# Kernel optimization log

Hardware: AMD Instinct MI355X
Metric: run time of the kernel (lower is better)

The kernel has to match this reference:

```python
import math
import jax, jax.numpy as jnp
import numpy as np

NUM_LAYERS = 2  # init arg num_layers
MASK_FILL = 1e-10  # non-standard fill used by the original (not -inf)


def _pos_encoding(L, D):
    # Matches torch PositionalEncoding buffer (dropout is identity in eval).
    pos = np.arange(L, dtype=np.float32)[:, None]
    div = np.exp(np.arange(0, D, 2, dtype=np.float32) * (-math.log(10000.0) / D))
    pe = np.zeros((L, D), dtype=np.float32)
    pe[:, 0::2] = np.sin(pos * div)
    pe[:, 1::2] = np.cos(pos * div)
    return jnp.asarray(pe)


def setup_inputs() -> dict:
    B, L, D = 1024, 100, 512
    key = jax.random.key(0)
    ks = jax.random.split(key, 6)
    x = jax.random.normal(ks[0], (B, L, D), dtype=jnp.float32)
    text_len = jax.random.randint(ks[1], (B,), 1, L + 1)  # in [1, L]
    scale = 1.0 / np.sqrt(2 * D)  # stand-in for orthogonal init
    W_r = jax.random.normal(ks[2], (2 * D, D), dtype=jnp.float32) * scale
    W_u = jax.random.normal(ks[3], (2 * D, D), dtype=jnp.float32) * scale
    W_o = jax.random.normal(ks[4], (2 * D, D), dtype=jnp.float32) * scale
    b = jnp.zeros((D,), dtype=jnp.float32)
    return {"x": x, "text_len": text_len, "W_r": W_r, "b_r": b,
            "W_u": W_u, "b_u": b, "W_o": W_o, "b_o": b}


def reference(x, text_len, W_r, b_r, W_u, b_u, W_o, b_o):
    B, L, D = x.shape
    pe = _pos_encoding(L, D)  # [L, D]
    valid = jnp.arange(L)[None, :] < text_len[:, None]          # [B, L]
    mask = valid[:, :, None] & valid[:, None, :]                 # [B, L, L]
    for _ in range(NUM_LAYERS):
        xp = x + pe  # PE (dropout identity in eval), applied to both sides
        score = jnp.einsum('bld,bmd->blm', xp, xp)               # [B, L, L]
        score = jnp.where(mask, score, MASK_FILL)
        attn = jax.nn.softmax(score, axis=2)
        message = jnp.einsum('blm,bmd->bld', attn, x)            # [B, L, D]
        # ConvGRU cell (prev_state = x): gates are Linear on last dim
        si = jnp.concatenate([message, x], axis=-1)              # [B, L, 2D]
        update = jax.nn.sigmoid(si @ W_u + b_u)
        reset = jax.nn.sigmoid(si @ W_r + b_r)
        so = jnp.concatenate([message, x * reset], axis=-1)
        cand = jnp.tanh(so @ W_o + b_o)
        x = x * (1.0 - update) + cand * update
    # mean_with_lens pooling
    lenf = text_len.astype(x.dtype)
    seq_emb = jnp.sum(x * valid[:, :, None].astype(x.dtype), axis=1) / lenf[:, None]
    return x, seq_emb
```

## Files before the change

kernel.cpp:

```cpp
#include <hip/hip_runtime.h>
#include <hip/hip_bf16.h>

#define B_ 1024
#define L_ 100
#define D_ 512
#define LP 128
#define ROWS (B_*L_)
#define XELEMS ((size_t)ROWS*D_)
#define HB 512
#define HR (HB*L_)
#define CATW 1536

typedef __attribute__((ext_vector_type(8))) short short8;
typedef __attribute__((ext_vector_type(4))) float f32x4;
typedef unsigned long long ull_t;

__device__ __forceinline__ short f2bf(float f) {
    __hip_bfloat16 h = __float2bfloat16(f);
    return *reinterpret_cast<short*>(&h);
}
__device__ __forceinline__ float bf2f(short s) {
    __hip_bfloat16 h = *reinterpret_cast<__hip_bfloat16*>(&s);
    return __bfloat162float(h);
}

__device__ __forceinline__ void cp16(void* lds, const void* g) {
    __builtin_amdgcn_global_load_lds(
        (const __attribute__((address_space(1))) unsigned int*)g,
        (__attribute__((address_space(3))) unsigned int*)lds, 16, 0, 0);
}

__device__ __forceinline__ f32x4 mfma16(short8 a, short8 b, f32x4 c) {
    return __builtin_amdgcn_mfma_f32_16x16x32_bf16(a, b, c, 0, 0, 0);
}

__global__ __launch_bounds__(256) void pe_kernel(float* __restrict__ pe) {
    int idx = blockIdx.x * 256 + threadIdx.x;
    if (idx >= L_ * D_) return;
    int l = idx >> 9;
    int d = idx & 511;
    int i = d >> 1;
    float div = __expf((float)(2 * i) * (-9.210340371976184f / 512.0f));
    float angle = (float)l * div;
    pe[idx] = (d & 1) ? __cosf(angle) : __sinf(angle);
}

__global__ __launch_bounds__(256) void cvtw_kernel(const float* __restrict__ W,
                                                   __hip_bfloat16* __restrict__ Wt) {
    int idx = blockIdx.x * 256 + threadIdx.x;
    int n = idx >> 10, k = idx & 1023;
    Wt[idx] = __float2bfloat16(W[(size_t)k * D_ + n]);
}

template<int BF16IN>
__global__ __launch_bounds__(256) void attn_kernel(
    const float* __restrict__ x, const float* __restrict__ pe,
    const int* __restrict__ text_len, __hip_bfloat16* __restrict__ xTb,
    __hip_bfloat16* __restrict__ cat, int bh)
{
    __shared__ __align__(16) char sm[16384 + 32768];
    char* XP = sm;
    char* P  = sm + 16384;
    const int bl = blockIdx.x;
    const int b = bh * HB + bl;
    const int len = text_len[b];
    const int tid = threadIdx.x;
    const int w = tid >> 6, g = (tid >> 4) & 3, cl = tid & 15;
    const int lane = tid & 63;
    const float* xb = x + (size_t)b * L_ * D_;
    __hip_bfloat16* xTg = xTb + (size_t)bl * D_ * LP;

    {
        __hip_bfloat16 (*t)[66] = (__hip_bfloat16 (*)[66])XP;
        for (int d0 = 0; d0 < D_; d0 += 64) {
            for (int l0 = 0; l0 < LP; l0 += 64) {
                int l_loc = tid >> 2;
                int dq = tid & 3;
                int l = l0 + l_loc;
                #pragma unroll
                for (int i = 0; i < 4; ++i) {
                    int d_loc = (dq * 4 + i) * 4;
                    if constexpr (BF16IN) {
                        ull_t u = 0ull;
                        if (l < L_)
                            u = *(const ull_t*)(cat + ((size_t)bl * L_ + l) * CATW + 512 + d0 + d_loc);
                        union { ull_t u; short s[4]; } pk;
                        pk.u = u;
                        t[l_loc][d_loc + 0] = *reinterpret_cast<__hip_bfloat16*>(&pk.s[0]);
                        t[l_loc][d_loc + 1] = *reinterpret_cast<__hip_bfloat16*>(&pk.s[1]);
                        t[l_loc][d_loc + 2] = *reinterpret_cast<__hip_bfloat16*>(&pk.s[2]);
                        t[l_loc][d_loc + 3] = *reinterpret_cast<__hip_bfloat16*>(&pk.s[3]);
                    } else {
                        float4 v = (l < L_) ? *(const float4*)(xb + (size_t)l * D_ + d0 + d_loc)
                                            : make_float4(0.f, 0.f, 0.f, 0.f);
                        short s0 = f2bf(v.x), s1 = f2bf(v.y), s2 = f2bf(v.z), s3 = f2bf(v.w);
                        t[l_loc][d_loc + 0] = *reinterpret_cast<__hip_bfloat16*>(&s0);
                        t[l_loc][d_loc + 1] = *reinterpret_cast<__hip_bfloat16*>(&s1);
                        t[l_loc][d_loc + 2] = *reinterpret_cast<__hip_bfloat16*>(&s2);
                        t[l_loc][d_loc + 3] = *reinterpret_cast<__hip_bfloat16*>(&s3);
                        if (l < L_) {
                            union { short s[4]; ull_t u; } pk;
                            pk.s[0] = s0; pk.s[1] = s1; pk.s[2] = s2; pk.s[3] = s3;
                            *(ull_t*)(cat + ((size_t)bl * L_ + l) * CATW + 512 + d0 + d_loc) = pk.u;
                        }
                    }
                }
                __syncthreads();
                int dl = tid >> 2, seg = tid & 3;
                short8 lo, hi;
                #pragma unroll
                for (int j = 0; j < 8; ++j) {
                    __hip_bfloat16 a = t[seg * 16 + j][dl];
                    __hip_bfloat16 bswap = t[seg * 16 + 8 + j][dl];
                    lo[j] = *reinterpret_cast<short*>(&a);
                    hi[j] = *reinterpret_cast<short*>(&bswap);
                }
                __hip_bfloat16* dst = xTg + (size_t)(d0 + dl) * LP + l0 + seg * 16;
                *(short8*)dst = lo;
                *(short8*)(dst + 8) = hi;
                __syncthreads();
            }
        }
    }

    f32x4 accS[2][8];
    const f32x4 fz = {0.f, 0.f, 0.f, 0.f};
    #pragma unroll
    for (int i = 0; i < 2; ++i)
        #pragma unroll
        for (int j = 0; j < 8; ++j) accS[i][j] = fz;

    for (int kc = 0; kc < D_; kc += 64) {
        #pragma unroll
        for (int i = 0; i < 4; ++i) {
            int c = tid + 256 * i;
            int row = c >> 3, k8d = c & 7;
            int k = kc + 8 * (k8d ^ (row & 7));
            if (row < L_) {
                const float* pp = pe + row * D_ + k;
                float4 b0 = *(const float4*)pp, b1 = *(const float4*)(pp + 4);
                short8 xv = *(const short8*)(cat + ((size_t)bl * L_ + row) * CATW + 512 + k);
                short8 h;
                h[0] = f2bf(bf2f(xv[0]) + b0.x); h[1] = f2bf(bf2f(xv[1]) + b0.y);
                h[2] = f2bf(bf2f(xv[2]) + b0.z); h[3] = f2bf(bf2f(xv[3]) + b0.w);
                h[4] = f2bf(bf2f(xv[4]) + b1.x); h[5] = f2bf(bf2f(xv[5]) + b1.y);
                h[6] = f2bf(bf2f(xv[6]) + b1.z); h[7] = f2bf(bf2f(xv[7]) + b1.w);
                *(short8*)(XP + row * 128 + 16 * k8d) = h;
            } else if (kc == 0) {
                short8 h;
                #pragma unroll
                for (int q = 0; q < 8; ++q) h[q] = 0;
                *(short8*)(XP + row * 128 + 16 * k8d) = h;
            }
        }
        __syncthreads();
        #pragma unroll
        for (int kt = 0; kt < 2; ++kt) {
            short8 a[2];
            #pragma unroll
            for (int rt = 0; rt < 2; ++rt) {
                int r = 32 * w + 16 * rt + cl;
                a[rt] = *(const short8*)(XP + r * 128 + ((16 * g + 64 * kt) ^ ((r & 7) << 4)));
            }
            #pragma unroll
            for (int ct = 0; ct < 8; ++ct) {
                int m = 16 * ct + cl;
                short8 bb = *(const short8*)(XP + m * 128 + ((16 * g + 64 * kt) ^ ((m & 7) << 4)));
                accS[0][ct] = mfma16(a[0], bb, accS[0][ct]);
                accS[1][ct] = mfma16(a[1], bb, accS[1][ct]);
            }
        }
        __syncthreads();
    }

    #pragma unroll
    for (int rt = 0; rt < 2; ++rt) {
        #pragma unroll
        for (int reg = 0; reg < 4; ++reg) {
            int rl = 32 * w + 16 * rt + 4 * g + reg;
            float s[8];
            #pragma unroll
            for (int ct = 0; ct < 8; ++ct) {
                int col = 16 * ct + cl;
                float v = accS[rt][ct][reg];
                if (col >= L_) v = -INFINITY;
                else if (rl >= len || col >= len) v = 1e-10f;
                s[ct] = v;
            }
            float mx = s[0];
            #pragma unroll
            for (int ct = 1; ct < 8; ++ct) mx = fmaxf(mx, s[ct]);
            mx = fmaxf(mx, __shfl_xor(mx, 1));
            mx = fmaxf(mx, __shfl_xor(mx, 2));
            mx = fmaxf(mx, __shfl_xor(mx, 4));
            mx = fmaxf(mx, __shfl_xor(mx, 8));
            float e[8], sum = 0.f;
            #pragma unroll
            for (int ct = 0; ct < 8; ++ct) { e[ct] = __expf(s[ct] - mx); sum += e[ct]; }
            sum += __shfl_xor(sum, 1);
            sum += __shfl_xor(sum, 2);
            sum += __shfl_xor(sum, 4);
            sum += __shfl_xor(sum, 8);
            float inv = 1.f / sum;
            #pragma unroll
            for (int ct = 0; ct < 8; ++ct) {
                int col = 16 * ct + cl;
                *(short*)(P + rl * 256 + ((col * 2) ^ ((rl & 7) << 4))) = f2bf(e[ct] * inv);
            }
        }
    }

    const __hip_bfloat16* xT = xTg;
    char* TW = XP + w * 4096;
    for (int nc = 0; nc < 4; ++nc) {
        f32x4 accM[2][8];
        #pragma unroll
        for (int i = 0; i < 2; ++i)
            #pragma unroll
            for (int j = 0; j < 8; ++j) accM[i][j] = fz;
        #pragma unroll
        for (int kt = 0; kt < 4; ++kt) {
            short8 a[2];
            #pragma unroll
            for (int rt = 0; rt < 2; ++rt) {
                int r = 32 * w + 16 * rt + cl;
                a[rt] = *(const short8*)(P + r * 256 + ((16 * g + 64 * kt) ^ ((r & 7) << 4)));
            }
            #pragma unroll
            for (int nt = 0; nt < 8; ++nt) {
                int d = nc * 128 + nt * 16 + cl;
                short8 bb = *(const short8*)(xT + (size_t)d * LP + 8 * g + 32 * kt);
                accM[0][nt] = mfma16(a[0], bb, accM[0][nt]);
                accM[1][nt] = mfma16(a[1], bb, accM[1][nt]);
            }
        }
        #pragma unroll
        for (int rt = 0; rt < 2; ++rt) {
            #pragma unroll
            for (int nt = 0; nt < 8; ++nt) {
                #pragma unroll
                for (int reg = 0; reg < 4; ++reg) {
                    int rloc = 4 * g + reg;
                    int cc = nt * 16 + cl;
                    *(short*)(TW + rloc * 256 + ((2 * cc) ^ ((rloc & 15) << 4))) =
                        f2bf(accM[rt][nt][reg]);
                }
            }
            asm volatile("s_waitcnt lgkmcnt(0)" ::: "memory");
            __builtin_amdgcn_sched_barrier(0);
            {
                int r4 = lane >> 4;
                int c16 = lane & 15;
                #pragma unroll
                for (int it = 0; it < 4; ++it) {
                    int rloc = it * 4 + r4;
                    int rl = 32 * w + 16 * rt + rloc;
                    if (rl < L_) {
                        int byte = (c16 * 16) ^ ((rloc & 15) << 4);
                        short8 v = *(const short8*)(TW + rloc * 256 + byte);
                        int d = nc * 128 + c16 * 8;
                        *(short8*)(cat + ((size_t)bl * L_ + rl) * CATW + d) = v;
                    }
                }
            }
            asm volatile("s_waitcnt lgkmcnt(0)" ::: "memory");
            __builtin_amdgcn_sched_barrier(0);
        }
    }
}

template<int MODE, int LAST>
__global__ __launch_bounds__(256) void gemm_gates(
    const __hip_bfloat16* __restrict__ cat,
    const __hip_bfloat16* __restrict__ Wt,
    const float* __restrict__ bias0, const float* __restrict__ bias1,
    __hip_bfloat16* __restrict__ upd,
    __hip_bfloat16* __restrict__ catw,
    float* __restrict__ xdst)
{
    __shared__ __align__(16) char sm[49152];
    const int tid = threadIdx.x;
    const int w = tid >> 6, g = (tid >> 4) & 3, cl = tid & 15;
    const int wr = w >> 1, wc = w & 1;
    constexpr int NY = (MODE == 0) ? 8 : 4;
    const int cpx = gridDim.x >> 3;
    const int bid = blockIdx.x;
    const int swz = (bid & 7) * cpx + (bid >> 3);
    const int bx = swz / NY, by = swz % NY;
    const size_t R0 = (size_t)bx * 128;
    const int col0 = by * 128;

    int srow[2], skoff[2];
    #pragma unroll
    for (int i = 0; i < 2; ++i) {
        int p = tid + 256 * i;
        int R = p >> 3, s = p & 7;
        int u = s ^ (R & 7);
        srow[i] = 2 * R + (u >> 2);
        skoff[i] = (u & 3) * 16;
    }

    auto stage = [&](int t, char* buf) {
        const int kc = t * 32;
        const int ka = (MODE == 0) ? kc : (t < 16 ? kc : kc + 512);
        #pragma unroll
        for (int i = 0; i < 2; ++i) {
            int p = tid + 256 * i;
            const char* gA = (const char*)(cat + (R0 + srow[i]) * CATW + ka) + skoff[i];
            cp16(buf + p * 16, gA);
        }
        #pragma unroll
        for (int i = 0; i < 2; ++i) {
            int p = tid + 256 * i;
            const char* gB = (const char*)(Wt + (size_t)(col0 + srow[i]) * 1024 + kc) + skoff[i];
            cp16(buf + 8192 + p * 16, gB);
        }
    };

    f32x4 acc[4][4];
    const f32x4 fz = {0.f, 0.f, 0.f, 0.f};
    #pragma unroll
    for (int i = 0; i < 4; ++i)
        #pragma unroll
        for (int j = 0; j < 4; ++j) acc[i][j] = fz;

    stage(0, sm);
    stage(1, sm + 16384);
    #pragma unroll 1
    for (int t = 0; t < 32; ++t) {
        char* buf = sm + 16384 * (t % 3);
        if (t < 31) asm volatile("s_waitcnt vmcnt(4)" ::: "memory");
        else        asm volatile("s_waitcnt vmcnt(0)" ::: "memory");
        __builtin_amdgcn_sched_barrier(0);
        __builtin_amdgcn_s_barrier();
        if (t + 2 < 32)
            stage(t + 2, sm + 16384 * ((t + 2) % 3));

        short8 aA[4], bb[4];
        #pragma unroll
        for (int rt = 0; rt < 4; ++rt) {
            int r = wr * 64 + rt * 16 + cl;
            int Rr = r >> 1;
            int sA = (((r & 1) << 2) + g) ^ (Rr & 7);
            aA[rt] = *(const short8*)(buf + Rr * 128 + 16 * sA);
        }
        #pragma unroll
        for (int ct = 0; ct < 4; ++ct) {
            int n = wc * 64 + ct * 16 + cl;
            int Rn = n >> 1;
            int sB = (((n & 1) << 2) + g) ^ (Rn & 7);
            bb[ct] = *(const short8*)(buf + 8192 + Rn * 128 + 16 * sB);
        }
        __builtin_amdgcn_s_setprio(1);
        #pragma unroll
        for (int rt = 0; rt < 4; ++rt)
            #pragma unroll
            for (int ct = 0; ct < 4; ++ct)
                acc[rt][ct] = mfma16(aA[rt], bb[ct], acc[rt][ct]);
        __builtin_amdgcn_s_setprio(0);
    }

    char* T = sm;
    #pragma unroll
    for (int ct = 0; ct < 4; ++ct) {
        int c = wc * 64 + ct * 16 + cl;
        int colg = col0 + c;
        float bb = (MODE == 0) ? ((col0 < 512) ? bias0[colg] : bias1[colg - 512])
                               : bias0[colg];
        #pragma unroll
        for (int rt = 0; rt < 4; ++rt) {
            #pragma unroll
            for (int reg = 0; reg < 4; ++reg) {
                int r = wr * 64 + rt * 16 + g * 4 + reg;
                float z = acc[rt][ct][reg] + bb;
                float v;
                if (MODE == 0) v = 1.f / (1.f + __expf(-z));
                else           v = 1.f - 2.f * __fdividef(1.f, 1.f + __expf(2.f * z));
                *(short*)(T + r * 256 + ((2 * c) ^ ((r & 15) << 4))) = f2bf(v);
            }
        }
    }
    __syncthreads();
    {
        const int rr = tid >> 4;
        const int c16 = tid & 15;
        #pragma unroll
        for (int it = 0; it < 8; ++it) {
            int r = it * 16 + rr;
            const size_t grow = R0 + r;
            int byte = (c16 * 16) ^ ((r & 15) << 4);
            short8 v = *(const short8*)(T + r * 256 + byte);
            int colg = col0 + c16 * 8;
            if (MODE == 0) {
                if (col0 < 512) {
                    *(short8*)(upd + grow * D_ + colg) = v;
                } else {
                    int c2 = colg - 512;
                    short8 xv = *(const short8*)(cat + grow * CATW + 512 + c2);
                    short8 o;
                    #pragma unroll
                    for (int q = 0; q < 8; ++q)
                        o[q] = f2bf(bf2f(xv[q]) * bf2f(v[q]));
                    *(short8*)(catw + grow * CATW + 1024 + c2) = o;
                }
            } else {
                short8 uv = *(const short8*)(upd + grow * D_ + colg);
                short8 xv = *(const short8*)(cat + grow * CATW + 512 + colg);
                if (LAST) {
                    float o[8];
                    #pragma unroll
                    for (int q = 0; q < 8; ++q) {
                        float u = bf2f(uv[q]), x_ = bf2f(xv[q]), cd = bf2f(v[q]);
                        o[q] = x_ + u * (cd - x_);
                    }
                    *(float4*)(xdst + grow * D_ + colg)     = make_float4(o[0], o[1], o[2], o[3]);
                    *(float4*)(xdst + grow * D_ + colg + 4) = make_float4(o[4], o[5], o[6], o[7]);
                } else {
                    short8 o;
                    #pragma unroll
                    for (int q = 0; q < 8; ++q) {
                        float u = bf2f(uv[q]), x_ = bf2f(xv[q]), cd = bf2f(v[q]);
                        o[q] = f2bf(x_ + u * (cd - x_));
                    }
                    *(short8*)(catw + grow * CATW + 512 + colg) = o;
                }
            }
        }
    }
}

__global__ __launch_bounds__(256) void pool_kernel(
    const float* __restrict__ x, const int* __restrict__ text_len,
    float* __restrict__ seq)
{
    int b = blockIdx.x;
    int len = text_len[b];
    float invlen = 1.f / (float)len;
    const float* xb = x + (size_t)b * L_ * D_;
    for (int d = threadIdx.x; d < D_; d += 256) {
        float acc = 0.f;
        for (int l = 0; l < len; ++l)
            acc += xb[(size_t)l * D_ + d];
        seq[(size_t)b * D_ + d] = acc * invlen;
    }
}

extern "C" void kernel_launch(void* const* d_in, const int* in_sizes, int n_in,
                              void* d_out, int out_size, void* d_ws, size_t ws_size,
                              hipStream_t stream) {
    const float* x_in = (const float*)d_in[0];
    const int* text_len = (const int*)d_in[1];
    const float* W_r = (const float*)d_in[2];
    const float* b_r = (const float*)d_in[3];
    const float* W_u = (const float*)d_in[4];
    const float* b_u = (const float*)d_in[5];
    const float* W_o = (const float*)d_in[6];
    const float* b_o = (const float*)d_in[7];

    float* xwork = (float*)d_out;
    float* seq_out = (float*)d_out + XELEMS;

    char* ws = (char*)d_ws;
    float* pe            = (float*)ws;
    __hip_bfloat16* WurT = (__hip_bfloat16*)(ws + 204800);
    __hip_bfloat16* WoT  = (__hip_bfloat16*)(ws + 2301952);
    __hip_bfloat16* cat  = (__hip_bfloat16*)(ws + 3350528);
    char* unionR         = ws + 160636928ull;
    __hip_bfloat16* xTb  = (__hip_bfloat16*)unionR;
    __hip_bfloat16* upd  = (__hip_bfloat16*)unionR;

    pe_kernel<<<(L_ * D_ + 255) / 256, 256, 0, stream>>>(pe);
    cvtw_kernel<<<2048, 256, 0, stream>>>(W_u, WurT);
    cvtw_kernel<<<2048, 256, 0, stream>>>(W_r, WurT + 512 * 1024);
    cvtw_kernel<<<2048, 256, 0, stream>>>(W_o, WoT);

    for (int h = 0; h < 2; ++h) {
        float* xdh = xwork + (size_t)h * HR * D_;
        attn_kernel<0><<<HB, 256, 0, stream>>>(x_in, pe, text_len, xTb, cat, h);
        gemm_gates<0, 0><<<3200, 256, 0, stream>>>(cat, WurT, b_u, b_r, upd, cat, nullptr);
        gemm_gates<1, 0><<<1600, 256, 0, stream>>>(cat, WoT, b_o, nullptr, upd, cat, nullptr);
        attn_kernel<1><<<HB, 256, 0, stream>>>(nullptr, pe, text_len, xTb, cat, h);
        gemm_gates<0, 0><<<3200, 256, 0, stream>>>(cat, WurT, b_u, b_r, upd, cat, nullptr);
        gemm_gates<1, 1><<<1600, 256, 0, stream>>>(cat, WoT, b_o, nullptr, upd, cat, xdh);
    }
    pool_kernel<<<B_, 256, 0, stream>>>(xwork, text_len, seq_out);
}
```

Baseline: 1.458 ms.

## Split attention kernel into two blocks per batch over query-row halves

```diff
diff --git a/kernel.cpp b/kernel.cpp
--- a/kernel.cpp
+++ b/kernel.cpp
@@ -58,10 +58,11 @@
     const int* __restrict__ text_len, __hip_bfloat16* __restrict__ xTb,
     __hip_bfloat16* __restrict__ cat, int bh)
 {
-    __shared__ __align__(16) char sm[16384 + 32768];
+    __shared__ __align__(16) char sm[16384 + 16384];
     char* XP = sm;
     char* P  = sm + 16384;
-    const int bl = blockIdx.x;
+    const int bl = blockIdx.x >> 1;
+    const int qb = blockIdx.x & 1;
     const int b = bh * HB + bl;
     const int len = text_len[b];
     const int tid = threadIdx.x;
@@ -123,12 +124,10 @@
         }
     }
 
-    f32x4 accS[2][8];
+    f32x4 accS[8];
     const f32x4 fz = {0.f, 0.f, 0.f, 0.f};
     #pragma unroll
-    for (int i = 0; i < 2; ++i)
-        #pragma unroll
-        for (int j = 0; j < 8; ++j) accS[i][j] = fz;
+    for (int j = 0; j < 8; ++j) accS[j] = fz;
 
     for (int kc = 0; kc < D_; kc += 64) {
         #pragma unroll
@@ -156,116 +155,99 @@
         __syncthreads();
         #pragma unroll
         for (int kt = 0; kt < 2; ++kt) {
-            short8 a[2];
-            #pragma unroll
-            for (int rt = 0; rt < 2; ++rt) {
-                int r = 32 * w + 16 * rt + cl;
-                a[rt] = *(const short8*)(XP + r * 128 + ((16 * g + 64 * kt) ^ ((r & 7) << 4)));
-            }
+            int r = qb * 64 + 16 * w + cl;
+            short8 a = *(const short8*)(XP + r * 128 + ((16 * g + 64 * kt) ^ ((r & 7) << 4)));
             #pragma unroll
             for (int ct = 0; ct < 8; ++ct) {
                 int m = 16 * ct + cl;
                 short8 bb = *(const short8*)(XP + m * 128 + ((16 * g + 64 * kt) ^ ((m & 7) << 4)));
-                accS[0][ct] = mfma16(a[0], bb, accS[0][ct]);
-                accS[1][ct] = mfma16(a[1], bb, accS[1][ct]);
+                accS[ct] = mfma16(a, bb, accS[ct]);
             }
         }
         __syncthreads();
     }
 
     #pragma unroll
-    for (int rt = 0; rt < 2; ++rt) {
-        #pragma unroll
-        for (int reg = 0; reg < 4; ++reg) {
-            int rl = 32 * w + 16 * rt + 4 * g + reg;
-            float s[8];
-            #pragma unroll
-            for (int ct = 0; ct < 8; ++ct) {
-                int col = 16 * ct + cl;
-                float v = accS[rt][ct][reg];
-                if (col >= L_) v = -INFINITY;
-                else if (rl >= len || col >= len) v = 1e-10f;
-                s[ct] = v;
-            }
-            float mx = s[0];
-            #pragma unroll
-            for (int ct = 1; ct < 8; ++ct) mx = fmaxf(mx, s[ct]);
-            mx = fmaxf(mx, __shfl_xor(mx, 1));
-            mx = fmaxf(mx, __shfl_xor(mx, 2));
-            mx = fmaxf(mx, __shfl_xor(mx, 4));
-            mx = fmaxf(mx, __shfl_xor(mx, 8));
-            float e[8], sum = 0.f;
-            #pragma unroll
-            for (int ct = 0; ct < 8; ++ct) { e[ct] = __expf(s[ct] - mx); sum += e[ct]; }
-            sum += __shfl_xor(sum, 1);
-            sum += __shfl_xor(sum, 2);
-            sum += __shfl_xor(sum, 4);
-            sum += __shfl_xor(sum, 8);
-            float inv = 1.f / sum;
-            #pragma unroll
-            for (int ct = 0; ct < 8; ++ct) {
-                int col = 16 * ct + cl;
-                *(short*)(P + rl * 256 + ((col * 2) ^ ((rl & 7) << 4))) = f2bf(e[ct] * inv);
-            }
+    for (int reg = 0; reg < 4; ++reg) {
+        int rlq = 16 * w + 4 * g + reg;
+        int rl = qb * 64 + rlq;
+        float s[8];
+        #pragma unroll
+        for (int ct = 0; ct < 8; ++ct) {
+            int col = 16 * ct + cl;
+            float v = accS[ct][reg];
+            if (col >= L_) v = -INFINITY;
+            else if (rl >= len || col >= len) v = 1e-10f;
+            s[ct] = v;
+        }
+        float mx = s[0];
+        #pragma unroll
+        for (int ct = 1; ct < 8; ++ct) mx = fmaxf(mx, s[ct]);
+        mx = fmaxf(mx, __shfl_xor(mx, 1));
+        mx = fmaxf(mx, __shfl_xor(mx, 2));
+        mx = fmaxf(mx, __shfl_xor(mx, 4));
+        mx = fmaxf(mx, __shfl_xor(mx, 8));
+        float e[8], sum = 0.f;
+        #pragma unroll
+        for (int ct = 0; ct < 8; ++ct) { e[ct] = __expf(s[ct] - mx); sum += e[ct]; }
+        sum += __shfl_xor(sum, 1);
+        sum += __shfl_xor(sum, 2);
+        sum += __shfl_xor(sum, 4);
+        sum += __shfl_xor(sum, 8);
+        float inv = 1.f / sum;
+        #pragma unroll
+        for (int ct = 0; ct < 8; ++ct) {
+            int col = 16 * ct + cl;
+            *(short*)(P + rlq * 256 + ((col * 2) ^ ((rlq & 7) << 4))) = f2bf(e[ct] * inv);
         }
     }
 
     const __hip_bfloat16* xT = xTg;
     char* TW = XP + w * 4096;
     for (int nc = 0; nc < 4; ++nc) {
-        f32x4 accM[2][8];
-        #pragma unroll
-        for (int i = 0; i < 2; ++i)
-            #pragma unroll
-            for (int j = 0; j < 8; ++j) accM[i][j] = fz;
+        f32x4 accM[8];
+        #pragma unroll
+        for (int j = 0; j < 8; ++j) accM[j] = fz;
         #pragma unroll
         for (int kt = 0; kt < 4; ++kt) {
-            short8 a[2];
-            #pragma unroll
-            for (int rt = 0; rt < 2; ++rt) {
-                int r = 32 * w + 16 * rt + cl;
-                a[rt] = *(const short8*)(P + r * 256 + ((16 * g + 64 * kt) ^ ((r & 7) << 4)));
-            }
+            int r = 16 * w + cl;
+            short8 a = *(const short8*)(P + r * 256 + ((16 * g + 64 * kt) ^ ((r & 7) << 4)));
             #pragma unroll
             for (int nt = 0; nt < 8; ++nt) {
                 int d = nc * 128 + nt * 16 + cl;
                 short8 bb = *(const short8*)(xT + (size_t)d * LP + 8 * g + 32 * kt);
-                accM[0][nt] = mfma16(a[0], bb, accM[0][nt]);
-                accM[1][nt] = mfma16(a[1], bb, accM[1][nt]);
-            }
-        }
-        #pragma unroll
-        for (int rt = 0; rt < 2; ++rt) {
-            #pragma unroll
-            for (int nt = 0; nt < 8; ++nt) {
-                #pragma unroll
-                for (int reg = 0; reg < 4; ++reg) {
-                    int rloc = 4 * g + reg;
-                    int cc = nt * 16 + cl;
-                    *(short*)(TW + rloc * 256 + ((2 * cc) ^ ((rloc & 15) << 4))) =
-                        f2bf(accM[rt][nt][reg]);
+                accM[nt] = mfma16(a, bb, accM[nt]);
+            }
+        }
+        #pragma unroll
+        for (int nt = 0; nt < 8; ++nt) {
+            #pragma unroll
+            for (int reg = 0; reg < 4; ++reg) {
+                int rloc = 4 * g + reg;
+                int cc = nt * 16 + cl;
+                *(short*)(TW + rloc * 256 + ((2 * cc) ^ ((rloc & 15) << 4))) =
+                    f2bf(accM[nt][reg]);
+            }
+        }
+        asm volatile("s_waitcnt lgkmcnt(0)" ::: "memory");
+        __builtin_amdgcn_sched_barrier(0);
+        {
+            int r4 = lane >> 4;
+            int c16 = lane & 15;
+            #pragma unroll
+            for (int it = 0; it < 4; ++it) {
+                int rloc = it * 4 + r4;
+                int rl = qb * 64 + 16 * w + rloc;
+                if (rl < L_) {
+                    int byte = (c16 * 16) ^ ((rloc & 15) << 4);
+                    short8 v = *(const short8*)(TW + rloc * 256 + byte);
+                    int d = nc * 128 + c16 * 8;
+                    *(short8*)(cat + ((size_t)bl * L_ + rl) * CATW + d) = v;
                 }
             }
-            asm volatile("s_waitcnt lgkmcnt(0)" ::: "memory");
-            __builtin_amdgcn_sched_barrier(0);
-            {
-                int r4 = lane >> 4;
-                int c16 = lane & 15;
-                #pragma unroll
-                for (int it = 0; it < 4; ++it) {
-                    int rloc = it * 4 + r4;
-                    int rl = 32 * w + 16 * rt + rloc;
-                    if (rl < L_) {
-                        int byte = (c16 * 16) ^ ((rloc & 15) << 4);
-                        short8 v = *(const short8*)(TW + rloc * 256 + byte);
-                        int d = nc * 128 + c16 * 8;
-                        *(short8*)(cat + ((size_t)bl * L_ + rl) * CATW + d) = v;
-                    }
-                }
-            }
-            asm volatile("s_waitcnt lgkmcnt(0)" ::: "memory");
-            __builtin_amdgcn_sched_barrier(0);
-        }
+        }
+        asm volatile("s_waitcnt lgkmcnt(0)" ::: "memory");
+        __builtin_amdgcn_sched_barrier(0);
     }
 }
 
@@ -476,10 +458,10 @@
 
     for (int h = 0; h < 2; ++h) {
         float* xdh = xwork + (size_t)h * HR * D_;
-        attn_kernel<0><<<HB, 256, 0, stream>>>(x_in, pe, text_len, xTb, cat, h);
+        attn_kernel<0><<<HB * 2, 256, 0, stream>>>(x_in, pe, text_len, xTb, cat, h);
         gemm_gates<0, 0><<<3200, 256, 0, stream>>>(cat, WurT, b_u, b_r, upd, cat, nullptr);
         gemm_gates<1, 0><<<1600, 256, 0, stream>>>(cat, WoT, b_o, nullptr, upd, cat, nullptr);
-        attn_kernel<1><<<HB, 256, 0, stream>>>(nullptr, pe, text_len, xTb, cat, h);
+        attn_kernel<1><<<HB * 2, 256, 0, stream>>>(nullptr, pe, text_len, xTb, cat, h);
         gemm_gates<0, 0><<<3200, 256, 0, stream>>>(cat, WurT, b_u, b_r, upd, cat, nullptr);
         gemm_gates<1, 1><<<1600, 256, 0, stream>>>(cat, WoT, b_o, nullptr, upd, cat, xdh);
     }
```

Result: slower. 1.677 ms (+15.0%).
